# Optimization experiments

Measured on AMD Instinct MI355X. Metric: run time of the kernel, lower is better.

The kernel has to match this reference:

```python
import jax, jax.numpy as jnp
import numpy as np

N_HARMONIC = 8
FRAME_SHIFT = 240
SR = 24000
ALPHA = 0.1
SIGMA = 0.003
B = 32
N_FRAMES = 500


def setup_inputs() -> dict:
    key = jax.random.key(0)
    k1, k2, k3, k4 = jax.random.split(key, 4)
    u = jax.random.uniform(k1, (B, N_FRAMES), dtype=jnp.float32)
    f0s = jnp.where(u < 0.1, 0.0, 80.0 + u * 320.0)
    # random phase per harmonic in [-pi, 0], phi[0] = 0 (matches torch init)
    phi = jax.random.uniform(k2, (N_HARMONIC,), dtype=jnp.float32) * (-np.pi)
    phi = phi.at[0].set(0.0)
    amplitude = jax.random.normal(k3, (N_HARMONIC + 1,), dtype=jnp.float32)
    # per-harmonic gaussian noise N(0, sigma) at sample rate
    noise = SIGMA * jax.random.normal(
        k4, (N_HARMONIC, B, N_FRAMES * FRAME_SHIFT), dtype=jnp.float32)
    return {"f0s": f0s, "phi": phi, "amplitude": amplitude, "noise": noise}


def reference(f0s, phi, amplitude, noise):
    # upsample frame-rate f0 to sample rate: [B, n_frames] -> [B, T]
    f0_up = jnp.repeat(f0s, FRAME_SHIFT, axis=1)
    # cumsum is linear in harmonic index: compute once, scale by (i+1)
    cs = jnp.cumsum(2.0 * np.pi * f0_up / SR, axis=1)            # [B, T]
    k = jnp.arange(1, N_HARMONIC + 1, dtype=f0s.dtype)           # [H]
    sin_all = jnp.sin(k[:, None, None] * cs[None] + phi[:, None, None])  # [H, B, T]
    pos = (f0_up > 0).astype(f0s.dtype)                          # [B, T]
    zero = (f0_up == 0).astype(f0s.dtype)                        # [B, T]
    # excitation per harmonic: voiced -> alpha*sin + noise; unvoiced -> scaled noise
    exc = (ALPHA * sin_all + noise) * pos + zero * (ALPHA / (3.0 * SIGMA)) * noise
    out = jnp.tanh(jnp.einsum('h,hbt->bt', amplitude[:N_HARMONIC], exc)
                   + amplitude[N_HARMONIC])
    return out
```

## Files before the change

kernel.cpp:

```cpp
#include <hip/hip_runtime.h>
#include <math.h>

constexpr int   BB    = 32;
constexpr int   NF    = 500;
constexpr int   FS    = 240;
constexpr int   TT    = NF * FS;
constexpr int   HH    = 8;
constexpr float ALPHA = 0.1f;

constexpr int SPT = 8;
constexpr int BLK = 256;

__device__ __forceinline__ float sin_rev(float fr) {
#if __has_builtin(__builtin_amdgcn_sinf)
    return __builtin_amdgcn_sinf(fr);
#else
    return __sinf(fr * 6.28318530717958647692f);
#endif
}

__device__ __forceinline__ float tanh_fast(float x) {
    const float e = __expf(2.0f * x);
#if __has_builtin(__builtin_amdgcn_rcpf)
    const float r = __builtin_amdgcn_rcpf(e + 1.0f);
#else
    const float r = 1.0f / (e + 1.0f);
#endif
    return fmaf(-2.0f, r, 1.0f);
}

__global__ __launch_bounds__(BLK) void synth_fused(const float* __restrict__ f0s,
                                                   const float* __restrict__ phi,
                                                   const float* __restrict__ amp,
                                                   const float* __restrict__ noise,
                                                   float* __restrict__ out) {
    const int b   = blockIdx.y;
    const int tid = threadIdx.x;

    __shared__ float2 sfr[NF];

    const int t     = (blockIdx.x * BLK + tid) * SPT;
    const bool valid = (t < TT);
    const int tc    = valid ? t : (TT - SPT);
    const int f     = tc / FS;
    const int j     = tc - f * FS;
    const size_t base = (size_t)b * TT + tc;

    float4 n0[HH], n1[HH];
#pragma unroll
    for (int h = 0; h < HH; ++h) {
        const float4* p = reinterpret_cast<const float4*>(
            noise + (size_t)h * (BB * (size_t)TT) + base);
        n0[h] = p[0];
        n1[h] = p[1];
    }

    if (tid < 64) {
        const int lane = tid;
        const float  TWO_PI_F = 6.28318530717958647692f;
        const double INV_2PI  = 0.15915494309189533576;

        double d[8];
        double sum = 0.0;
#pragma unroll
        for (int i = 0; i < 8; ++i) {
            const int fr = lane * 8 + i;
            const float f0   = (fr < NF) ? f0s[b * NF + fr] : 0.0f;
            const float dphi = (TWO_PI_F * f0) / 24000.0f;
            d[i] = (double)dphi * INV_2PI;
            sum += d[i];
        }

        const double mine = sum * 240.0;
        double run = mine;
        for (int delta = 1; delta < 64; delta <<= 1) {
            const double o = __shfl_up(run, delta, 64);
            if (lane >= delta) run += o;
        }
        double acc = run - mine;

#pragma unroll
        for (int i = 0; i < 8; ++i) {
            const int fr = lane * 8 + i;
            if (fr < NF) {
                const double fx = acc - rint(acc);
                sfr[fr] = make_float2((float)fx, (float)d[i]);
            }
            acc += d[i] * 240.0;
        }
    }
    __syncthreads();

    const float2 fd = sfr[f];
    const float  dr = fd.y;
    const bool   voiced = (dr > 0.0f);

    float cs[SPT];
    cs[0] = fd.x + (float)(j + 1) * dr;
#pragma unroll
    for (int e = 1; e < SPT; ++e) cs[e] = cs[e - 1] + dr;

    const float INV2PIf = 0.15915494309189533576f;

    float sdot[SPT], ndot[SPT], kcs[SPT];
#pragma unroll
    for (int e = 0; e < SPT; ++e) { sdot[e] = 0.f; ndot[e] = 0.f; kcs[e] = 0.f; }

#pragma unroll
    for (int h = 0; h < HH; ++h) {
        const float a  = amp[h];
        const float ph = phi[h] * INV2PIf;

        ndot[0] = fmaf(a, n0[h].x, ndot[0]);
        ndot[1] = fmaf(a, n0[h].y, ndot[1]);
        ndot[2] = fmaf(a, n0[h].z, ndot[2]);
        ndot[3] = fmaf(a, n0[h].w, ndot[3]);
        ndot[4] = fmaf(a, n1[h].x, ndot[4]);
        ndot[5] = fmaf(a, n1[h].y, ndot[5]);
        ndot[6] = fmaf(a, n1[h].z, ndot[6]);
        ndot[7] = fmaf(a, n1[h].w, ndot[7]);

#pragma unroll
        for (int e = 0; e < SPT; ++e) {
            kcs[e] += cs[e];
            const float r  = kcs[e] + ph;
            const float fx = r - rintf(r);
            sdot[e] = fmaf(a, sin_rev(fx), sdot[e]);
        }
    }

    const float a8 = amp[HH];
    const float UV = (float)(0.1 / (3.0 * 0.003));

    float tmp[SPT];
#pragma unroll
    for (int e = 0; e < SPT; ++e) {
        const float x = voiced ? fmaf(ALPHA, sdot[e], ndot[e]) : UV * ndot[e];
        tmp[e] = tanh_fast(x + a8);
    }

    if (valid) {
        float4* ov = reinterpret_cast<float4*>(out + base);
        ov[0] = make_float4(tmp[0], tmp[1], tmp[2], tmp[3]);
        ov[1] = make_float4(tmp[4], tmp[5], tmp[6], tmp[7]);
    }
}

extern "C" void kernel_launch(void* const* d_in, const int* in_sizes, int n_in,
                              void* d_out, int out_size, void* d_ws, size_t ws_size,
                              hipStream_t stream) {
    const float* f0s   = (const float*)d_in[0];
    const float* phi   = (const float*)d_in[1];
    const float* amp   = (const float*)d_in[2];
    const float* noise = (const float*)d_in[3];
    float* out = (float*)d_out;

    const int blocks_x = (TT / SPT + BLK - 1) / BLK;
    dim3 grid(blocks_x, BB);
    synth_fused<<<grid, BLK, 0, stream>>>(f0s, phi, amp, noise, out);
}
```

Measured before the change: 30.93 us.

## Parallelize frame-phase scan across all waves and use nontemporal noise loads/stores

The per-frame phase prefix scan now runs on all four waves, two frames per thread, with a cross-wave offset combined through shared memory, instead of on one wave handling eight frames each. Noise loads are moved after the scan and issued as nontemporal loads per harmonic, and outputs use nontemporal stores. Harmonic phase is computed as k*cs+phi with one fma instead of a running sum. The goal is to cut the serial scan latency and cache pollution on streaming data, but delaying the noise loads until after the scan loses the overlap that previously hid memory latency behind it.

```diff
diff --git a/kernel.cpp b/kernel.cpp
--- a/kernel.cpp
+++ b/kernel.cpp
@@ -10,6 +10,8 @@
 
 constexpr int SPT = 8;
 constexpr int BLK = 256;
+
+typedef float f32x4 __attribute__((ext_vector_type(4)));
 
 __device__ __forceinline__ float sin_rev(float fr) {
 #if __has_builtin(__builtin_amdgcn_sinf)
@@ -34,62 +36,60 @@
                                                    const float* __restrict__ amp,
                                                    const float* __restrict__ noise,
                                                    float* __restrict__ out) {
-    const int b   = blockIdx.y;
-    const int tid = threadIdx.x;
+    const int b    = blockIdx.y;
+    const int tid  = threadIdx.x;
+    const int lane = tid & 63;
+    const int wv   = tid >> 6;
 
     __shared__ float2 sfr[NF];
+    __shared__ double wtot[BLK / 64];
 
-    const int t     = (blockIdx.x * BLK + tid) * SPT;
-    const bool valid = (t < TT);
-    const int tc    = valid ? t : (TT - SPT);
-    const int f     = tc / FS;
-    const int j     = tc - f * FS;
-    const size_t base = (size_t)b * TT + tc;
-
-    float4 n0[HH], n1[HH];
-#pragma unroll
-    for (int h = 0; h < HH; ++h) {
-        const float4* p = reinterpret_cast<const float4*>(
-            noise + (size_t)h * (BB * (size_t)TT) + base);
-        n0[h] = p[0];
-        n1[h] = p[1];
-    }
-
-    if (tid < 64) {
-        const int lane = tid;
+    {
         const float  TWO_PI_F = 6.28318530717958647692f;
         const double INV_2PI  = 0.15915494309189533576;
 
-        double d[8];
-        double sum = 0.0;
-#pragma unroll
-        for (int i = 0; i < 8; ++i) {
-            const int fr = lane * 8 + i;
-            const float f0   = (fr < NF) ? f0s[b * NF + fr] : 0.0f;
-            const float dphi = (TWO_PI_F * f0) / 24000.0f;
-            d[i] = (double)dphi * INV_2PI;
-            sum += d[i];
+        const int fi = 2 * tid;
+        double d0 = 0.0, d1 = 0.0;
+        if (fi < NF) {
+            const float dphi = (TWO_PI_F * f0s[b * NF + fi]) / 24000.0f;
+            d0 = (double)dphi * INV_2PI;
+        }
+        if (fi + 1 < NF) {
+            const float dphi = (TWO_PI_F * f0s[b * NF + fi + 1]) / 24000.0f;
+            d1 = (double)dphi * INV_2PI;
         }
 
-        const double mine = sum * 240.0;
-        double run = mine;
+        const double s = (d0 + d1) * 240.0;
+        double run = s;
         for (int delta = 1; delta < 64; delta <<= 1) {
             const double o = __shfl_up(run, delta, 64);
             if (lane >= delta) run += o;
         }
-        double acc = run - mine;
+        if (lane == 63) wtot[wv] = run;
+        __syncthreads();
 
-#pragma unroll
-        for (int i = 0; i < 8; ++i) {
-            const int fr = lane * 8 + i;
-            if (fr < NF) {
-                const double fx = acc - rint(acc);
-                sfr[fr] = make_float2((float)fx, (float)d[i]);
+        double woff = 0.0;
+        for (int w2 = 0; w2 < wv; ++w2) woff += wtot[w2];
+        double pref = woff + (run - s);
+
+        if (fi < NF) {
+            const double fx0 = pref - rint(pref);
+            sfr[fi] = make_float2((float)fx0, (float)d0);
+            if (fi + 1 < NF) {
+                const double p1  = pref + d0 * 240.0;
+                const double fx1 = p1 - rint(p1);
+                sfr[fi + 1] = make_float2((float)fx1, (float)d1);
             }
-            acc += d[i] * 240.0;
         }
+        __syncthreads();
     }
-    __syncthreads();
+
+    const int t = (blockIdx.x * BLK + tid) * SPT;
+    if (t >= TT) return;
+
+    const int f = t / FS;
+    const int j = t - f * FS;
+    const size_t base = (size_t)b * TT + t;
 
     const float2 fd = sfr[f];
     const float  dr = fd.y;
@@ -102,28 +102,33 @@
 
     const float INV2PIf = 0.15915494309189533576f;
 
-    float sdot[SPT], ndot[SPT], kcs[SPT];
+    float sdot[SPT], ndot[SPT];
 #pragma unroll
-    for (int e = 0; e < SPT; ++e) { sdot[e] = 0.f; ndot[e] = 0.f; kcs[e] = 0.f; }
+    for (int e = 0; e < SPT; ++e) { sdot[e] = 0.f; ndot[e] = 0.f; }
 
 #pragma unroll
     for (int h = 0; h < HH; ++h) {
         const float a  = amp[h];
         const float ph = phi[h] * INV2PIf;
+        const float kf = (float)(h + 1);
 
-        ndot[0] = fmaf(a, n0[h].x, ndot[0]);
-        ndot[1] = fmaf(a, n0[h].y, ndot[1]);
-        ndot[2] = fmaf(a, n0[h].z, ndot[2]);
-        ndot[3] = fmaf(a, n0[h].w, ndot[3]);
-        ndot[4] = fmaf(a, n1[h].x, ndot[4]);
-        ndot[5] = fmaf(a, n1[h].y, ndot[5]);
-        ndot[6] = fmaf(a, n1[h].z, ndot[6]);
-        ndot[7] = fmaf(a, n1[h].w, ndot[7]);
+        const f32x4* p = reinterpret_cast<const f32x4*>(
+            noise + (size_t)h * (BB * (size_t)TT) + base);
+        const f32x4 m0 = __builtin_nontemporal_load(p);
+        const f32x4 m1 = __builtin_nontemporal_load(p + 1);
+
+        ndot[0] = fmaf(a, m0.x, ndot[0]);
+        ndot[1] = fmaf(a, m0.y, ndot[1]);
+        ndot[2] = fmaf(a, m0.z, ndot[2]);
+        ndot[3] = fmaf(a, m0.w, ndot[3]);
+        ndot[4] = fmaf(a, m1.x, ndot[4]);
+        ndot[5] = fmaf(a, m1.y, ndot[5]);
+        ndot[6] = fmaf(a, m1.z, ndot[6]);
+        ndot[7] = fmaf(a, m1.w, ndot[7]);
 
 #pragma unroll
         for (int e = 0; e < SPT; ++e) {
-            kcs[e] += cs[e];
-            const float r  = kcs[e] + ph;
+            const float r  = fmaf(kf, cs[e], ph);
             const float fx = r - rintf(r);
             sdot[e] = fmaf(a, sin_rev(fx), sdot[e]);
         }
@@ -139,11 +144,11 @@
         tmp[e] = tanh_fast(x + a8);
     }
 
-    if (valid) {
-        float4* ov = reinterpret_cast<float4*>(out + base);
-        ov[0] = make_float4(tmp[0], tmp[1], tmp[2], tmp[3]);
-        ov[1] = make_float4(tmp[4], tmp[5], tmp[6], tmp[7]);
-    }
+    f32x4* ov = reinterpret_cast<f32x4*>(out + base);
+    f32x4 o0; o0.x = tmp[0]; o0.y = tmp[1]; o0.z = tmp[2]; o0.w = tmp[3];
+    f32x4 o1; o1.x = tmp[4]; o1.y = tmp[5]; o1.z = tmp[6]; o1.w = tmp[7];
+    __builtin_nontemporal_store(o0, ov);
+    __builtin_nontemporal_store(o1, ov + 1);
 }
 
 extern "C" void kernel_launch(void* const* d_in, const int* in_sizes, int n_in,
```

Result: slower. 34.12 us (+10.3%).
